# Kernel optimization log

Measured on AMD Instinct MI355X. Metric: run time of the kernel, lower is better.

## Reference

```python
import jax, jax.numpy as jnp
import numpy as np

OUT = 7          # output_size
SR = 2           # sampling_ratio
IMG = 512.0      # image size (512, 512)
CANON_SCALE = 224.0
CANON_LVL = 4.0
LVL_MIN, LVL_MAX = 2, 6  # strides 4..64


def roi_align_level(feat, rois, scale):
    """torchvision roi_align (aligned=False) for all rois on one level.
    feat: [B,C,H,W], rois: [B,N,4] in image coords. Returns [B,N,C,7,7]."""
    B, C, H, W = feat.shape
    N = rois.shape[1]
    x1 = rois[..., 0] * scale
    y1 = rois[..., 1] * scale
    x2 = rois[..., 2] * scale
    y2 = rois[..., 3] * scale
    roi_w = jnp.maximum(x2 - x1, 1.0)
    roi_h = jnp.maximum(y2 - y1, 1.0)
    bin_w = roi_w / OUT
    bin_h = roi_h / OUT
    # 14 sample coordinates per axis: 7 bins x 2 samples, offset (i+0.5)/2 within bin
    grid = (jnp.arange(OUT, dtype=feat.dtype)[:, None]
            + (jnp.arange(SR, dtype=feat.dtype)[None, :] + 0.5) / SR).reshape(-1)  # [14]
    py = y1[..., None] + grid * bin_h[..., None]   # [B,N,14]
    px = x1[..., None] + grid * bin_w[..., None]   # [B,N,14]
    yy = py[..., :, None]                          # [B,N,14,1]
    xx = px[..., None, :]                          # [B,N,1,14]
    valid = (yy >= -1.0) & (yy <= H) & (xx >= -1.0) & (xx <= W)  # [B,N,14,14]
    y = jnp.clip(yy, 0.0, H - 1)
    x = jnp.clip(xx, 0.0, W - 1)
    y0f = jnp.floor(y)
    x0f = jnp.floor(x)
    ly = y - y0f   # [B,N,14,1]
    lx = x - x0f   # [B,N,1,14]
    y0 = y0f.astype(jnp.int32)
    x0 = x0f.astype(jnp.int32)
    y1i = jnp.minimum(y0 + 1, H - 1)
    x1i = jnp.minimum(x0 + 1, W - 1)

    flat = feat.reshape(B, C, H * W)

    def gather(yi, xi):
        idx = (yi * W + xi).reshape(B, -1)                     # [B, N*14*14]
        g = jax.vmap(lambda f, i: f[:, i])(flat, idx)          # [B, C, N*14*14]
        return g.reshape(B, C, N, SR * OUT, SR * OUT)

    w00 = ((1 - ly) * (1 - lx))[:, None]  # [B,1,N,14,14]
    w01 = ((1 - ly) * lx)[:, None]
    w10 = (ly * (1 - lx))[:, None]
    w11 = (ly * lx)[:, None]
    val = (gather(y0, x0) * w00 + gather(y0, x1i) * w01
           + gather(y1i, x0) * w10 + gather(y1i, x1i) * w11)
    val = val * valid[:, None].astype(feat.dtype)
    # average the SRxSR samples within each bin
    out = val.reshape(B, C, N, OUT, SR, OUT, SR).mean(axis=(4, 6))  # [B,C,N,7,7]
    return out.transpose(0, 2, 1, 3, 4)  # [B,N,C,7,7]


def setup_inputs() -> dict:
    key = jax.random.key(0)
    ks = jax.random.split(key, 6)
    B, C, N = 4, 256, 256
    feats = {}
    for lvl, hw in enumerate([128, 64, 32, 16, 8]):
        feats[f"feat{lvl}"] = jax.random.normal(ks[lvl], (B, C, hw, hw), dtype=jnp.float32)
    # random boxes inside the 512x512 image with x2>x1, y2>y1
    xy = jax.random.uniform(ks[5], (B, N, 2, 2), minval=0.0, maxval=IMG)
    lo = xy.min(axis=2)
    hi = xy.max(axis=2)
    rois = jnp.concatenate([lo, hi], axis=-1)  # [B,N,4] = (x1,y1,x2,y2)
    feats["rois"] = rois
    return feats


def reference(feat0, feat1, feat2, feat3, feat4, rois):
    B, N = rois.shape[0], rois.shape[1]
    feats = [feat0, feat1, feat2, feat3, feat4]
    scales = [0.25, 0.125, 0.0625, 0.03125, 0.015625]  # inferred from 128..8 vs 512
    # FPN level assignment (torchvision LevelMapper)
    area = (rois[..., 2] - rois[..., 0]) * (rois[..., 3] - rois[..., 1])
    lvl = jnp.floor(CANON_LVL + jnp.log2(jnp.sqrt(area) / CANON_SCALE + 1e-6))
    lvl = (jnp.clip(lvl, LVL_MIN, LVL_MAX) - LVL_MIN).astype(jnp.int32)  # [B,N] in 0..4
    # pool every roi on every level, then select its assigned level
    stacked = jnp.stack([roi_align_level(f, rois, s) for f, s in zip(feats, scales)],
                        axis=2)  # [B,N,5,C,7,7]
    sel = jnp.take_along_axis(stacked,
                              lvl[:, :, None, None, None, None].astype(jnp.int32),
                              axis=2)[:, :, 0]  # [B,N,C,7,7]
    B_, N_, C, _, _ = sel.shape
    return sel.reshape(B_ * N_, C, OUT, OUT)
```

## Files before the change

### kernel.cpp

```cpp
#include <hip/hip_runtime.h>

#define OUT 7
#define NB 4
#define NC 256
#define NN 256
#define EPR (NC * OUT * OUT)

typedef float nfloat4 __attribute__((ext_vector_type(4)));
typedef unsigned short nushort4 __attribute__((ext_vector_type(4)));

__device__ inline unsigned short f2bf(float f) {
    unsigned u = __builtin_bit_cast(unsigned, f);
    u += 0x7FFFu + ((u >> 16) & 1u);
    return (unsigned short)(u >> 16);
}

__device__ inline nfloat4 bf4_to_f4(nushort4 s) {
    nfloat4 r;
    r.x = __builtin_bit_cast(float, (unsigned)s.x << 16);
    r.y = __builtin_bit_cast(float, (unsigned)s.y << 16);
    r.z = __builtin_bit_cast(float, (unsigned)s.z << 16);
    r.w = __builtin_bit_cast(float, (unsigned)s.w << 16);
    return r;
}

__global__ __launch_bounds__(256) void transpose_all(
    const float* __restrict__ f0, const float* __restrict__ f1,
    const float* __restrict__ f2, const float* __restrict__ f3,
    const float* __restrict__ f4, unsigned short* __restrict__ T)
{
    __shared__ float tile[32][33];
    const int bx = blockIdx.x;

    const float* in; unsigned short* outp; int P, t, shp;
    if (bx < 16384)      { in = f0; outp = T;            P = 16384; t = bx;         shp = 9; }
    else if (bx < 20480) { in = f1; outp = T + 16777216; P = 4096;  t = bx - 16384; shp = 7; }
    else if (bx < 21504) { in = f2; outp = T + 20971520; P = 1024;  t = bx - 20480; shp = 5; }
    else if (bx < 21760) { in = f3; outp = T + 22020096; P = 256;   t = bx - 21504; shp = 3; }
    else                 { in = f4; outp = T + 22282240; P = 64;    t = bx - 21760; shp = 1; }

    const int pt   = t & ((1 << shp) - 1);
    const int rest = t >> shp;
    const int ct   = rest & 7;
    const int b    = rest >> 3;
    const int p0   = pt << 5;
    const int c0   = ct << 5;
    const int tx   = threadIdx.x & 7;
    const int ty   = threadIdx.x >> 3;

    const float* src = in + ((size_t)((b << 8) + c0 + ty)) * P + p0 + (tx << 2);
    nfloat4 v = *(const nfloat4*)src;
    tile[ty][tx * 4 + 0] = v.x;
    tile[ty][tx * 4 + 1] = v.y;
    tile[ty][tx * 4 + 2] = v.z;
    tile[ty][tx * 4 + 3] = v.w;
    __syncthreads();

    nushort4 w;
    w.x = f2bf(tile[4 * tx + 0][ty]);
    w.y = f2bf(tile[4 * tx + 1][ty]);
    w.z = f2bf(tile[4 * tx + 2][ty]);
    w.w = f2bf(tile[4 * tx + 3][ty]);
    unsigned short* dst = outp + ((size_t)b * P + p0 + ty) * NC + c0 + (tx << 2);
    *(nushort4*)dst = w;
}

__global__ __launch_bounds__(256, 3) void msroi_fast(
    const unsigned short* __restrict__ T, const float* __restrict__ rois,
    float* __restrict__ out)
{
    const int roi = blockIdx.x;
    const int tid = threadIdx.x;

    __shared__ float s_wyt[14], s_wyb[14], s_wxl[14], s_wxr[14];
    __shared__ int   s_yr0[14], s_yr1[14], s_x0[14], s_x1[14];
    __shared__ int   s_lvl;
    __shared__ __align__(16) float s_out[EPR];

    if (tid < 28) {
        const float rx1 = rois[roi * 4 + 0];
        const float ry1 = rois[roi * 4 + 1];
        const float rx2 = rois[roi * 4 + 2];
        const float ry2 = rois[roi * 4 + 3];

        float area = (rx2 - rx1) * (ry2 - ry1);
        float lf = floorf(4.0f + log2f(sqrtf(area) / 224.0f + 1e-6f));
        lf = fminf(fmaxf(lf, 2.0f), 6.0f);
        int lvl = (int)lf - 2;
        if (tid == 0) s_lvl = lvl;

        float scale = 1.0f / (float)(4 << lvl);
        int   W     = 128 >> lvl;

        float x1 = rx1 * scale, y1 = ry1 * scale;
        float x2 = rx2 * scale, y2 = ry2 * scale;
        float rw = fmaxf(x2 - x1, 1.0f);
        float rh = fmaxf(y2 - y1, 1.0f);
        float bw = rw / (float)OUT;
        float bh = rh / (float)OUT;

        bool isx = (tid >= 14);
        int  g   = isx ? tid - 14 : tid;
        float gv = ((float)g + 0.5f) * 0.5f;
        float p  = isx ? (x1 + gv * bw) : (y1 + gv * bh);

        float v = (p >= -1.0f && p <= (float)W) ? 1.0f : 0.0f;
        float pc  = fminf(fmaxf(p, 0.0f), (float)(W - 1));
        float p0f = floorf(pc);
        int   p0  = (int)p0f;
        int   p1  = min(p0 + 1, W - 1);
        float l   = pc - p0f;

        if (isx) {
            s_x0[g] = p0; s_x1[g] = p1;
            s_wxl[g] = v * (1.0f - l); s_wxr[g] = v * l;
        } else {
            s_yr0[g] = p0 * W; s_yr1[g] = p1 * W;
            s_wyt[g] = v * (1.0f - l); s_wyb[g] = v * l;
        }
    }
    __syncthreads();

    const int lvl = s_lvl;
    const int W   = 128 >> lvl;
    const int POS = W * W;
    const int off_tab[5] = {0, 16777216, 20971520, 22020096, 22282240};
    const int b   = roi >> 8;
    const int q   = tid >> 6;
    const int ch0 = (tid & 63) << 2;
    const unsigned short* base =
        T + (size_t)off_tab[lvl] + (size_t)b * POS * NC + ch0;

    auto make_pos = [&](int p, int* off, float* w) {
        const int oy = p / 7;
        const int ox = p - oy * 7;
        const int gy0 = oy * 2, gy1 = gy0 + 1;
        const int gx0 = ox * 2, gx1 = gx0 + 1;
        const float wt0 = s_wyt[gy0], wb0 = s_wyb[gy0];
        const float wt1 = s_wyt[gy1], wb1 = s_wyb[gy1];
        const int r00 = s_yr0[gy0], r01 = s_yr1[gy0];
        const int r10 = s_yr0[gy1], r11 = s_yr1[gy1];
        const float wl0 = s_wxl[gx0], wr0 = s_wxr[gx0];
        const float wl1 = s_wxl[gx1], wr1 = s_wxr[gx1];
        const int x00 = s_x0[gx0], x01 = s_x1[gx0];
        const int x10 = s_x0[gx1], x11 = s_x1[gx1];
        off[0]  = r00 + x00; w[0]  = wt0 * wl0;
        off[1]  = r00 + x01; w[1]  = wt0 * wr0;
        off[2]  = r01 + x00; w[2]  = wb0 * wl0;
        off[3]  = r01 + x01; w[3]  = wb0 * wr0;
        off[4]  = r00 + x10; w[4]  = wt0 * wl1;
        off[5]  = r00 + x11; w[5]  = wt0 * wr1;
        off[6]  = r01 + x10; w[6]  = wb0 * wl1;
        off[7]  = r01 + x11; w[7]  = wb0 * wr1;
        off[8]  = r10 + x00; w[8]  = wt1 * wl0;
        off[9]  = r10 + x01; w[9]  = wt1 * wr0;
        off[10] = r11 + x00; w[10] = wb1 * wl0;
        off[11] = r11 + x01; w[11] = wb1 * wr0;
        off[12] = r10 + x10; w[12] = wt1 * wl1;
        off[13] = r10 + x11; w[13] = wt1 * wr1;
        off[14] = r11 + x10; w[14] = wb1 * wl1;
        off[15] = r11 + x11; w[15] = wb1 * wr1;
    };

    int p_cur = min(q * 13, 48);
    int offA[16]; float wA[16];
    nushort4 L[16];
    make_pos(p_cur, offA, wA);
    #pragma unroll
    for (int k = 0; k < 16; ++k)
        L[k] = *(const nushort4*)&base[(size_t)offA[k] << 8];

    #pragma unroll
    for (int i = 0; i < 13; ++i) {
        const int p_nxt = min(q * 13 + i + 1, 48);
        int offB[16]; float wB[16];
        nushort4 M[16];
        if (i < 12) {
            make_pos(p_nxt, offB, wB);
            #pragma unroll
            for (int k = 0; k < 16; ++k)
                M[k] = *(const nushort4*)&base[(size_t)offB[k] << 8];
        }

        nfloat4 acc = {0.0f, 0.0f, 0.0f, 0.0f};
        #pragma unroll
        for (int k = 0; k < 16; ++k)
            acc += wA[k] * bf4_to_f4(L[k]);
        acc *= 0.25f;

        s_out[(ch0 + 0) * 49 + p_cur] = acc.x;
        s_out[(ch0 + 1) * 49 + p_cur] = acc.y;
        s_out[(ch0 + 2) * 49 + p_cur] = acc.z;
        s_out[(ch0 + 3) * 49 + p_cur] = acc.w;

        #pragma unroll
        for (int k = 0; k < 16; ++k) { L[k] = M[k]; wA[k] = wB[k]; }
        p_cur = p_nxt;
    }
    __syncthreads();

    float* ob = out + (size_t)roi * EPR;
    #pragma unroll
    for (int k = 0; k < 12; ++k) {
        const int f = (tid + (k << 8)) << 2;
        nfloat4 v = *(const nfloat4*)&s_out[f];
        __builtin_nontemporal_store(v, (nfloat4*)&ob[f]);
    }
    if (tid < 64) {
        const int f = (tid + 3072) << 2;
        nfloat4 v = *(const nfloat4*)&s_out[f];
        __builtin_nontemporal_store(v, (nfloat4*)&ob[f]);
    }
}

__global__ __launch_bounds__(256) void msroi_kernel(
    const float* __restrict__ f0, const float* __restrict__ f1,
    const float* __restrict__ f2, const float* __restrict__ f3,
    const float* __restrict__ f4, const float* __restrict__ rois,
    float* __restrict__ out)
{
    const int roi = blockIdx.y;
    const int tid = threadIdx.x;

    __shared__ float s_wyt[14], s_wyb[14];
    __shared__ float s_wxl[14], s_wxr[14];
    __shared__ int   s_oy0[14], s_oy1[14];
    __shared__ int   s_x0[14],  s_x1[14];
    __shared__ int   s_lvl;

    if (tid < 28) {
        const float rx1 = rois[roi * 4 + 0];
        const float ry1 = rois[roi * 4 + 1];
        const float rx2 = rois[roi * 4 + 2];
        const float ry2 = rois[roi * 4 + 3];

        float area = (rx2 - rx1) * (ry2 - ry1);
        float lf = floorf(4.0f + log2f(sqrtf(area) / 224.0f + 1e-6f));
        lf = fminf(fmaxf(lf, 2.0f), 6.0f);
        int lvl = (int)lf - 2;
        if (tid == 0) s_lvl = lvl;

        float scale = 1.0f / (float)(4 << lvl);
        int   HW    = 128 >> lvl;

        float x1 = rx1 * scale, y1 = ry1 * scale;
        float x2 = rx2 * scale, y2 = ry2 * scale;
        float rw = fmaxf(x2 - x1, 1.0f);
        float rh = fmaxf(y2 - y1, 1.0f);
        float bw = rw / (float)OUT;
        float bh = rh / (float)OUT;

        bool isx = (tid >= 14);
        int  g   = isx ? tid - 14 : tid;
        float gv = ((float)g + 0.5f) * 0.5f;
        float p  = isx ? (x1 + gv * bw) : (y1 + gv * bh);

        float v = (p >= -1.0f && p <= (float)HW) ? 1.0f : 0.0f;
        float pc  = fminf(fmaxf(p, 0.0f), (float)(HW - 1));
        float p0f = floorf(pc);
        int   p0  = (int)p0f;
        int   p1  = min(p0 + 1, HW - 1);
        float l   = pc - p0f;

        if (isx) {
            s_x0[g] = p0; s_x1[g] = p1;
            s_wxl[g] = v * (1.0f - l); s_wxr[g] = v * l;
        } else {
            s_oy0[g] = p0 * HW; s_oy1[g] = p1 * HW;
            s_wyt[g] = v * (1.0f - l); s_wyb[g] = v * l;
        }
    }
    __syncthreads();

    const int lvl = s_lvl;
    const int HW  = 128 >> lvl;
    const int HW2 = HW * HW;
    const float* f = (lvl == 0) ? f0 : (lvl == 1) ? f1 : (lvl == 2) ? f2
                     : (lvl == 3) ? f3 : f4;
    const int b = roi >> 8;

    const int e0 = blockIdx.x * 512 + tid;

    float acc[2];
    #pragma unroll
    for (int k = 0; k < 2; ++k) {
        const int e  = e0 + k * 256;
        const int ec = (e < EPR) ? e : 0;
        const int c  = ec / 49;
        const int s  = ec - 49 * c;
        const int oy = s / 7;
        const int ox = s - 7 * oy;

        const float* fp = f + (size_t)(b * NC + c) * (size_t)HW2;

        float a = 0.0f;
        #pragma unroll
        for (int iy = 0; iy < 2; ++iy) {
            const int gy = oy * 2 + iy;
            const float wt = s_wyt[gy], wb = s_wyb[gy];
            const int   o0 = s_oy0[gy], o1 = s_oy1[gy];
            #pragma unroll
            for (int ix = 0; ix < 2; ++ix) {
                const int gx = ox * 2 + ix;
                const float wl = s_wxl[gx], wr = s_wxr[gx];
                const int   x0 = s_x0[gx],  x1i = s_x1[gx];
                const float v00 = fp[o0 + x0];
                const float v01 = fp[o0 + x1i];
                const float v10 = fp[o1 + x0];
                const float v11 = fp[o1 + x1i];
                a += (wt * wl) * v00 + (wt * wr) * v01
                   + (wb * wl) * v10 + (wb * wr) * v11;
            }
        }
        acc[k] = a * 0.25f;
    }

    #pragma unroll
    for (int k = 0; k < 2; ++k) {
        const int e = e0 + k * 256;
        if (e < EPR)
            __builtin_nontemporal_store(acc[k], &out[(size_t)roi * EPR + e]);
    }
}

extern "C" void kernel_launch(void* const* d_in, const int* in_sizes, int n_in,
                              void* d_out, int out_size, void* d_ws, size_t ws_size,
                              hipStream_t stream) {
    const float* f0   = (const float*)d_in[0];
    const float* f1   = (const float*)d_in[1];
    const float* f2   = (const float*)d_in[2];
    const float* f3   = (const float*)d_in[3];
    const float* f4   = (const float*)d_in[4];
    const float* rois = (const float*)d_in[5];
    float* out = (float*)d_out;

    const size_t need = 22347776ull * 2ull;
    if (ws_size >= need) {
        unsigned short* T = (unsigned short*)d_ws;
        transpose_all<<<dim3(21824), dim3(256), 0, stream>>>(f0, f1, f2, f3, f4, T);
        msroi_fast<<<dim3(NB * NN), dim3(256), 0, stream>>>(T, rois, out);
    } else {
        dim3 grid((EPR + 511) / 512, NB * NN);
        dim3 block(256);
        msroi_kernel<<<grid, block, 0, stream>>>(f0, f1, f2, f3, f4, rois, out);
    }
}
```

Before: 171.2 us.

## Split ROI pooling into channel halves and batch transpose tiles per block

```diff
diff --git a/kernel.cpp b/kernel.cpp
--- a/kernel.cpp
+++ b/kernel.cpp
@@ -8,6 +8,7 @@
 
 typedef float nfloat4 __attribute__((ext_vector_type(4)));
 typedef unsigned short nushort4 __attribute__((ext_vector_type(4)));
+typedef unsigned short nushort2 __attribute__((ext_vector_type(2)));
 
 __device__ inline unsigned short f2bf(float f) {
     unsigned u = __builtin_bit_cast(unsigned, f);
@@ -15,13 +16,8 @@
     return (unsigned short)(u >> 16);
 }
 
-__device__ inline nfloat4 bf4_to_f4(nushort4 s) {
-    nfloat4 r;
-    r.x = __builtin_bit_cast(float, (unsigned)s.x << 16);
-    r.y = __builtin_bit_cast(float, (unsigned)s.y << 16);
-    r.z = __builtin_bit_cast(float, (unsigned)s.z << 16);
-    r.w = __builtin_bit_cast(float, (unsigned)s.w << 16);
-    return r;
+__device__ inline float bf2f(unsigned short s) {
+    return __builtin_bit_cast(float, (unsigned)s << 16);
 }
 
 __global__ __launch_bounds__(256) void transpose_all(
@@ -33,49 +29,56 @@
     const int bx = blockIdx.x;
 
     const float* in; unsigned short* outp; int P, t, shp;
-    if (bx < 16384)      { in = f0; outp = T;            P = 16384; t = bx;         shp = 9; }
-    else if (bx < 20480) { in = f1; outp = T + 16777216; P = 4096;  t = bx - 16384; shp = 7; }
-    else if (bx < 21504) { in = f2; outp = T + 20971520; P = 1024;  t = bx - 20480; shp = 5; }
-    else if (bx < 21760) { in = f3; outp = T + 22020096; P = 256;   t = bx - 21504; shp = 3; }
-    else                 { in = f4; outp = T + 22282240; P = 64;    t = bx - 21760; shp = 1; }
+    if (bx < 4096)      { in = f0; outp = T;            P = 16384; t = bx;        shp = 9; }
+    else if (bx < 5120) { in = f1; outp = T + 16777216; P = 4096;  t = bx - 4096; shp = 7; }
+    else if (bx < 5376) { in = f2; outp = T + 20971520; P = 1024;  t = bx - 5120; shp = 5; }
+    else if (bx < 5440) { in = f3; outp = T + 22020096; P = 256;   t = bx - 5376; shp = 3; }
+    else                { in = f4; outp = T + 22282240; P = 64;    t = bx - 5440; shp = 1; }
 
     const int pt   = t & ((1 << shp) - 1);
     const int rest = t >> shp;
-    const int ct   = rest & 7;
-    const int b    = rest >> 3;
+    const int cm   = rest & 1;
+    const int b    = rest >> 1;
     const int p0   = pt << 5;
-    const int c0   = ct << 5;
     const int tx   = threadIdx.x & 7;
     const int ty   = threadIdx.x >> 3;
 
-    const float* src = in + ((size_t)((b << 8) + c0 + ty)) * P + p0 + (tx << 2);
-    nfloat4 v = *(const nfloat4*)src;
-    tile[ty][tx * 4 + 0] = v.x;
-    tile[ty][tx * 4 + 1] = v.y;
-    tile[ty][tx * 4 + 2] = v.z;
-    tile[ty][tx * 4 + 3] = v.w;
-    __syncthreads();
-
-    nushort4 w;
-    w.x = f2bf(tile[4 * tx + 0][ty]);
-    w.y = f2bf(tile[4 * tx + 1][ty]);
-    w.z = f2bf(tile[4 * tx + 2][ty]);
-    w.w = f2bf(tile[4 * tx + 3][ty]);
-    unsigned short* dst = outp + ((size_t)b * P + p0 + ty) * NC + c0 + (tx << 2);
-    *(nushort4*)dst = w;
-}
-
-__global__ __launch_bounds__(256, 3) void msroi_fast(
+    #pragma unroll
+    for (int ct = 0; ct < 4; ++ct) {
+        const int c0 = (cm << 7) + (ct << 5);
+        const float* src = in + ((size_t)((b << 8) + c0 + ty)) * P + p0 + (tx << 2);
+        nfloat4 v = __builtin_nontemporal_load((const nfloat4*)src);
+        tile[ty][tx * 4 + 0] = v.x;
+        tile[ty][tx * 4 + 1] = v.y;
+        tile[ty][tx * 4 + 2] = v.z;
+        tile[ty][tx * 4 + 3] = v.w;
+        __syncthreads();
+
+        nushort4 w;
+        w.x = f2bf(tile[4 * tx + 0][ty]);
+        w.y = f2bf(tile[4 * tx + 1][ty]);
+        w.z = f2bf(tile[4 * tx + 2][ty]);
+        w.w = f2bf(tile[4 * tx + 3][ty]);
+        unsigned short* dst = outp + ((size_t)b * P + p0 + ty) * NC + c0 + (tx << 2);
+        *(nushort4*)dst = w;
+        __syncthreads();
+    }
+}
+
+__global__ __launch_bounds__(256, 5) void msroi_fast(
     const unsigned short* __restrict__ T, const float* __restrict__ rois,
     float* __restrict__ out)
 {
-    const int roi = blockIdx.x;
-    const int tid = threadIdx.x;
-
-    __shared__ float s_wyt[14], s_wyb[14], s_wxl[14], s_wxr[14];
-    __shared__ int   s_yr0[14], s_yr1[14], s_x0[14], s_x1[14];
+    const int roi   = blockIdx.x >> 1;
+    const int chunk = blockIdx.x & 1;
+    const int tid   = threadIdx.x;
+
+    __shared__ float s_wy[2][14];
+    __shared__ float s_wx[2][14];
+    __shared__ int   s_yr[2][14];
+    __shared__ int   s_xc[2][14];
     __shared__ int   s_lvl;
-    __shared__ __align__(16) float s_out[EPR];
+    __shared__ __align__(16) float s_out[128 * 49];
 
     if (tid < 28) {
         const float rx1 = rois[roi * 4 + 0];
@@ -112,11 +115,11 @@
         float l   = pc - p0f;
 
         if (isx) {
-            s_x0[g] = p0; s_x1[g] = p1;
-            s_wxl[g] = v * (1.0f - l); s_wxr[g] = v * l;
+            s_xc[0][g] = p0; s_xc[1][g] = p1;
+            s_wx[0][g] = v * (1.0f - l); s_wx[1][g] = v * l;
         } else {
-            s_yr0[g] = p0 * W; s_yr1[g] = p1 * W;
-            s_wyt[g] = v * (1.0f - l); s_wyb[g] = v * l;
+            s_yr[0][g] = p0 * W; s_yr[1][g] = p1 * W;
+            s_wy[0][g] = v * (1.0f - l); s_wy[1][g] = v * l;
         }
     }
     __syncthreads();
@@ -125,89 +128,78 @@
     const int W   = 128 >> lvl;
     const int POS = W * W;
     const int off_tab[5] = {0, 16777216, 20971520, 22020096, 22282240};
-    const int b   = roi >> 8;
-    const int q   = tid >> 6;
-    const int ch0 = (tid & 63) << 2;
+    const int b    = roi >> 8;
+    const int q    = tid >> 6;
+    const int cl   = (tid & 63) << 1;
     const unsigned short* base =
-        T + (size_t)off_tab[lvl] + (size_t)b * POS * NC + ch0;
-
-    auto make_pos = [&](int p, int* off, float* w) {
+        T + (size_t)off_tab[lvl] + (size_t)b * POS * NC + (chunk << 7) + cl;
+
+    auto make_off = [&](int p, int* off) {
         const int oy = p / 7;
         const int ox = p - oy * 7;
-        const int gy0 = oy * 2, gy1 = gy0 + 1;
-        const int gx0 = ox * 2, gx1 = gx0 + 1;
-        const float wt0 = s_wyt[gy0], wb0 = s_wyb[gy0];
-        const float wt1 = s_wyt[gy1], wb1 = s_wyb[gy1];
-        const int r00 = s_yr0[gy0], r01 = s_yr1[gy0];
-        const int r10 = s_yr0[gy1], r11 = s_yr1[gy1];
-        const float wl0 = s_wxl[gx0], wr0 = s_wxr[gx0];
-        const float wl1 = s_wxl[gx1], wr1 = s_wxr[gx1];
-        const int x00 = s_x0[gx0], x01 = s_x1[gx0];
-        const int x10 = s_x0[gx1], x11 = s_x1[gx1];
-        off[0]  = r00 + x00; w[0]  = wt0 * wl0;
-        off[1]  = r00 + x01; w[1]  = wt0 * wr0;
-        off[2]  = r01 + x00; w[2]  = wb0 * wl0;
-        off[3]  = r01 + x01; w[3]  = wb0 * wr0;
-        off[4]  = r00 + x10; w[4]  = wt0 * wl1;
-        off[5]  = r00 + x11; w[5]  = wt0 * wr1;
-        off[6]  = r01 + x10; w[6]  = wb0 * wl1;
-        off[7]  = r01 + x11; w[7]  = wb0 * wr1;
-        off[8]  = r10 + x00; w[8]  = wt1 * wl0;
-        off[9]  = r10 + x01; w[9]  = wt1 * wr0;
-        off[10] = r11 + x00; w[10] = wb1 * wl0;
-        off[11] = r11 + x01; w[11] = wb1 * wr0;
-        off[12] = r10 + x10; w[12] = wt1 * wl1;
-        off[13] = r10 + x11; w[13] = wt1 * wr1;
-        off[14] = r11 + x10; w[14] = wb1 * wl1;
-        off[15] = r11 + x11; w[15] = wb1 * wr1;
+        const int R[4] = { s_yr[0][2 * oy],     s_yr[1][2 * oy],
+                           s_yr[0][2 * oy + 1], s_yr[1][2 * oy + 1] };
+        const int C[4] = { s_xc[0][2 * ox],     s_xc[1][2 * ox],
+                           s_xc[0][2 * ox + 1], s_xc[1][2 * ox + 1] };
+        #pragma unroll
+        for (int a = 0; a < 4; ++a)
+            #pragma unroll
+            for (int c2 = 0; c2 < 4; ++c2)
+                off[a * 4 + c2] = R[a] + C[c2];
     };
 
     int p_cur = min(q * 13, 48);
-    int offA[16]; float wA[16];
-    nushort4 L[16];
-    make_pos(p_cur, offA, wA);
+    int offA[16];
+    nushort2 L[16], M[16];
+    make_off(p_cur, offA);
     #pragma unroll
     for (int k = 0; k < 16; ++k)
-        L[k] = *(const nushort4*)&base[(size_t)offA[k] << 8];
+        L[k] = *(const nushort2*)&base[(size_t)offA[k] << 8];
 
     #pragma unroll
     for (int i = 0; i < 13; ++i) {
         const int p_nxt = min(q * 13 + i + 1, 48);
-        int offB[16]; float wB[16];
-        nushort4 M[16];
         if (i < 12) {
-            make_pos(p_nxt, offB, wB);
+            int offB[16];
+            make_off(p_nxt, offB);
             #pragma unroll
             for (int k = 0; k < 16; ++k)
-                M[k] = *(const nushort4*)&base[(size_t)offB[k] << 8];
-        }
-
-        nfloat4 acc = {0.0f, 0.0f, 0.0f, 0.0f};
+                M[k] = *(const nushort2*)&base[(size_t)offB[k] << 8];
+        }
+
+        const int oy = p_cur / 7;
+        const int ox = p_cur - oy * 7;
+        const float WY[4] = { s_wy[0][2 * oy],     s_wy[1][2 * oy],
+                              s_wy[0][2 * oy + 1], s_wy[1][2 * oy + 1] };
+        const float WX[4] = { s_wx[0][2 * ox],     s_wx[1][2 * ox],
+                              s_wx[0][2 * ox + 1], s_wx[1][2 * ox + 1] };
+
+        float a0 = 0.0f, a1 = 0.0f;
         #pragma unroll
-        for (int k = 0; k < 16; ++k)
-            acc += wA[k] * bf4_to_f4(L[k]);
-        acc *= 0.25f;
-
-        s_out[(ch0 + 0) * 49 + p_cur] = acc.x;
-        s_out[(ch0 + 1) * 49 + p_cur] = acc.y;
-        s_out[(ch0 + 2) * 49 + p_cur] = acc.z;
-        s_out[(ch0 + 3) * 49 + p_cur] = acc.w;
+        for (int k = 0; k < 16; ++k) {
+            const float w = WY[k >> 2] * WX[k & 3];
+            a0 += w * bf2f(L[k].x);
+            a1 += w * bf2f(L[k].y);
+        }
+
+        s_out[(cl + 0) * 49 + p_cur] = a0 * 0.25f;
+        s_out[(cl + 1) * 49 + p_cur] = a1 * 0.25f;
 
         #pragma unroll
-        for (int k = 0; k < 16; ++k) { L[k] = M[k]; wA[k] = wB[k]; }
+        for (int k = 0; k < 16; ++k) L[k] = M[k];
         p_cur = p_nxt;
     }
     __syncthreads();
 
-    float* ob = out + (size_t)roi * EPR;
-    #pragma unroll
-    for (int k = 0; k < 12; ++k) {
+    float* ob = out + (size_t)roi * EPR + (chunk << 7) * 49;
+    #pragma unroll
+    for (int k = 0; k < 6; ++k) {
         const int f = (tid + (k << 8)) << 2;
         nfloat4 v = *(const nfloat4*)&s_out[f];
         __builtin_nontemporal_store(v, (nfloat4*)&ob[f]);
     }
-    if (tid < 64) {
-        const int f = (tid + 3072) << 2;
+    if (tid < 32) {
+        const int f = (tid + 1536) << 2;
         nfloat4 v = *(const nfloat4*)&s_out[f];
         __builtin_nontemporal_store(v, (nfloat4*)&ob[f]);
     }
@@ -337,8 +329,8 @@
     const size_t need = 22347776ull * 2ull;
     if (ws_size >= need) {
         unsigned short* T = (unsigned short*)d_ws;
-        transpose_all<<<dim3(21824), dim3(256), 0, stream>>>(f0, f1, f2, f3, f4, T);
-        msroi_fast<<<dim3(NB * NN), dim3(256), 0, stream>>>(T, rois, out);
+        transpose_all<<<dim3(5456), dim3(256), 0, stream>>>(f0, f1, f2, f3, f4, T);
+        msroi_fast<<<dim3(NB * NN * 2), dim3(256), 0, stream>>>(T, rois, out);
     } else {
         dim3 grid((EPR + 511) / 512, NB * NN);
         dim3 block(256);
```

Result: faster. 162.9 us (-4.8%).
